# Kernel tuning notes

Hardware: AMD Instinct MI355X
Metric: run time of the kernel (lower is better)

Reference implementation:

```python
import jax, jax.numpy as jnp
import numpy as np

N = 100_000      # total nodes across batch of graphs
E = 1_600_000    # total directed edges
D = 128          # input feature dim
H = 128          # hidden dim
OUT = 10         # output classes
B = 500          # number of graphs (200 nodes each)
L_MID = 3        # GIN layers after the first (num_layers-2)


def setup_inputs() -> dict:
    key = jax.random.key(0)
    ks = jax.random.split(key, 24)
    s = np.float32(1.0 / np.sqrt(H))
    f32 = jnp.float32
    inp = {
        'node_features': jax.random.normal(ks[0], (N, D), f32),
        'edge_src': jax.random.randint(ks[1], (E,), 0, N, jnp.int32),
        'edge_dst': jax.random.randint(ks[2], (E,), 0, N, jnp.int32),
        'graph_ids': (jnp.arange(N) // (N // B)).astype(jnp.int32),
        # GIN eps per layer (torch init: zeros)
        'eps': jnp.zeros((4,), f32),
        # pre MLP (input layer): Linear(D,H) -> BN -> ReLU -> Linear(H,H), then pre_batchnorm
        'pre_W1': jax.random.normal(ks[3], (D, H), f32) * s,
        'pre_b1': jnp.zeros((H,), f32),
        'pre_g1': jnp.ones((H,), f32),
        'pre_bt1': jnp.zeros((H,), f32),
        'pre_W2': jax.random.normal(ks[4], (H, H), f32) * s,
        'pre_b2': jnp.zeros((H,), f32),
        'pre_gout': jnp.ones((H,), f32),
        'pre_btout': jnp.zeros((H,), f32),
        # middle GIN layers (stacked over L_MID)
        'mlp_W1': jax.random.normal(ks[5], (L_MID, H, H), f32) * s,
        'mlp_b1': jnp.zeros((L_MID, H), f32),
        'mlp_g1': jnp.ones((L_MID, H), f32),
        'mlp_bt1': jnp.zeros((L_MID, H), f32),
        'mlp_W2': jax.random.normal(ks[6], (L_MID, H, H), f32) * s,
        'mlp_b2': jnp.zeros((L_MID, H), f32),
        'bn_g': jnp.ones((L_MID, H), f32),
        'bn_bt': jnp.zeros((L_MID, H), f32),
        # per-layer prediction heads
        'pred_W0': jax.random.normal(ks[7], (D, OUT), f32) * s,
        'pred_b0': jnp.zeros((OUT,), f32),
        'pred_W': jax.random.normal(ks[8], (4, H, OUT), f32) * s,
        'pred_b': jnp.zeros((4, OUT), f32),
    }
    return inp


def _mlp_bn(x, W1, b1, g1, bt1, W2, b2, go, bo):
    # MLP(num_mlp_layers=2): Linear -> BN(eval) -> ReLU -> Linear, then outer BN(eval) -> ReLU
    h = jax.nn.relu(g1 * (x @ W1 + b1) + bt1)
    h = h @ W2 + b2
    return jax.nn.relu(go * h + bo)


def reference(node_features, edge_src, edge_dst, graph_ids, eps,
              pre_W1, pre_b1, pre_g1, pre_bt1, pre_W2, pre_b2, pre_gout, pre_btout,
              mlp_W1, mlp_b1, mlp_g1, mlp_bt1, mlp_W2, mlp_b2, bn_g, bn_bt,
              pred_W0, pred_b0, pred_W, pred_b):
    def agg(h):
        # sparse Adj @ h via gather + segment_sum (sum neighbor pooling, learn_eps=True -> no self loops)
        return jax.ops.segment_sum(h[edge_src], edge_dst, num_segments=N)

    h = node_features
    reps = [h]
    pooled = agg(h) + (1.0 + eps[0]) * h
    h = _mlp_bn(pooled, pre_W1, pre_b1, pre_g1, pre_bt1, pre_W2, pre_b2, pre_gout, pre_btout)
    reps.append(h)
    for i in range(L_MID):
        pooled = agg(h) + (1.0 + eps[i + 1]) * h
        h = _mlp_bn(pooled, mlp_W1[i], mlp_b1[i], mlp_g1[i], mlp_bt1[i],
                    mlp_W2[i], mlp_b2[i], bn_g[i], bn_bt[i])
        reps.append(h)

    # graph-level sum pooling + per-layer linear heads (dropout off in eval)
    score = jax.ops.segment_sum(reps[0], graph_ids, num_segments=B) @ pred_W0 + pred_b0
    for k in range(4):
        score = score + jax.ops.segment_sum(reps[k + 1], graph_ids, num_segments=B) @ pred_W[k] + pred_b[k]
    return score  # [B, OUT]
```

## Files before the change

kernel.cpp:

```cpp
#include <hip/hip_runtime.h>
#include <hip/hip_bf16.h>

#define NN 100000
#define EE 1600000
#define HH 128
#define OUTC 10
#define BB 500
#define GSZ 200
#define LDA 136

#define NBKT 782
#define BCAP 2560
#define EPB 4096
#define NBUCKB 391
#define NTILE128 782

typedef float f32x4 __attribute__((ext_vector_type(4)));
typedef __bf16 bf16x8 __attribute__((ext_vector_type(8)));

__device__ __forceinline__ float b2f(unsigned short u){
    unsigned int x = ((unsigned int)u) << 16;
    return __builtin_bit_cast(float, x);
}
__device__ __forceinline__ unsigned short f2b(float f){
    __hip_bfloat16 h = __float2bfloat16(f);
    return __builtin_bit_cast(unsigned short, h);
}

__global__ __launch_bounds__(256) void k_setup(const int* __restrict__ src, const int* __restrict__ dst,
                                               int* __restrict__ bucket_cursor, unsigned int* __restrict__ ebuf,
                                               const float* __restrict__ x, unsigned short* __restrict__ hA,
                                               float* __restrict__ G,
                                               const float* __restrict__ preW1, const float* __restrict__ preW2,
                                               const float* __restrict__ mlpW1, const float* __restrict__ mlpW2,
                                               unsigned short* __restrict__ Wbf){
    __shared__ __align__(16) unsigned int sval[EPB];
    __shared__ unsigned short sbkt[EPB];
    __shared__ int shist[NBKT];
    int t = threadIdx.x;
    int bid = blockIdx.x;

    if (bid < NBUCKB){
        int e0 = bid * EPB;
        for (int i = t; i < NBKT; i += 256) shist[i] = 0;
        __syncthreads();
        for (int i = t; i < EPB; i += 256){
            int e = e0 + i;
            if (e < EE){
                int d = dst[e];
                int b = d >> 7;
                sval[i] = ((unsigned)src[e] << 7) | (unsigned)(d & 127);
                sbkt[i] = (unsigned short)b;
                atomicAdd(&shist[b], 1);
            } else {
                sbkt[i] = 0xffff;
            }
        }
        __syncthreads();
        for (int i = t; i < NBKT; i += 256){
            int c = shist[i];
            shist[i] = c ? atomicAdd(&bucket_cursor[i], c) : 0;
        }
        __syncthreads();
        for (int i = t; i < EPB; i += 256){
            unsigned short b = sbkt[i];
            if (b != 0xffff){
                int pos = atomicAdd(&shist[b], 1);
                if (pos < BCAP) ebuf[(int)b * BCAP + pos] = sval[i];
            }
        }
    } else if (bid < NBUCKB + BB){
        float* r0 = (float*)sval;
        float* r1 = r0 + 256;
        int g = bid - NBUCKB;
        int f2 = t & 63;
        int rg = t >> 6;
        if (t < 128){
            #pragma unroll
            for (int k = 1; k < 5; ++k) G[(size_t)k*BB*128 + g*128 + t] = 0.f;
        }
        float a0 = 0.f, a1 = 0.f;
        for (int i = rg; i < GSZ; i += 4){
            int node = g*GSZ + i;
            float2 v = *(const float2*)(x + (size_t)node*128 + f2*2);
            a0 += v.x; a1 += v.y;
            unsigned int o = (unsigned)f2b(v.x) | ((unsigned)f2b(v.y) << 16);
            ((unsigned int*)hA)[(size_t)node*64 + f2] = o;
        }
        r0[t] = a0; r1[t] = a1;
        __syncthreads();
        if (t < 64){
            float s0 = r0[t] + r0[t+64] + r0[t+128] + r0[t+192];
            float s1 = r1[t] + r1[t+64] + r1[t+128] + r1[t+192];
            float2 v; v.x = s0; v.y = s1;
            *(float2*)(G + g*128 + t*2) = v;
        }
    } else {
        int idx = (bid - NBUCKB - BB)*256 + t;
        int w = idx >> 14;
        int rem = idx & 16383;
        int e = rem & 7;
        int chunk = rem >> 3;
        int m = chunk & 15;
        int q = (chunk >> 4) & 3;
        int kk = (chunk >> 6) & 3;
        int j = chunk >> 8;
        int n = j*16 + m;
        int k = kk*32 + q*8 + e;
        const float* s;
        if      (w == 0) s = preW1;
        else if (w == 1) s = preW2;
        else if (w <  5) s = mlpW1 + (w-2)*16384;
        else             s = mlpW2 + (w-5)*16384;
        Wbf[idx] = f2b(s[k*128 + n]);
    }
}

__global__ __launch_bounds__(1024) void k_bscan(const int* __restrict__ bucket_cursor,
                                                int* __restrict__ bucket_base, int* __restrict__ row_ptr){
    __shared__ int tmp[1024];
    int t = threadIdx.x;
    int v = (t < NBKT) ? min(bucket_cursor[t], BCAP) : 0;
    tmp[t] = v; __syncthreads();
    for (int off = 1; off < 1024; off <<= 1){
        int a = (t >= off) ? tmp[t - off] : 0;
        __syncthreads();
        tmp[t] += a;
        __syncthreads();
    }
    if (t < NBKT) bucket_base[t + 1] = tmp[t];
    if (t == 0){ bucket_base[0] = 0; row_ptr[NN] = EE; }
}

__global__ __launch_bounds__(256) void k_csr(const int* __restrict__ bucket_cursor, const int* __restrict__ bucket_base,
                                             const unsigned int* __restrict__ ebuf,
                                             int* __restrict__ row_ptr, int* __restrict__ col){
    __shared__ int cnt[128];
    __shared__ int pfx[128];
    int b = blockIdx.x;
    int t = threadIdx.x;
    int c    = min(bucket_cursor[b], BCAP);
    int base = bucket_base[b];
    if (t < 128) cnt[t] = 0;
    __syncthreads();
    const unsigned int* eb = ebuf + (size_t)b * BCAP;
    for (int i = t; i < c; i += 256) atomicAdd(&cnt[eb[i] & 127], 1);
    __syncthreads();
    if (t == 0){
        int run = 0;
        for (int i = 0; i < 128; ++i){ pfx[i] = run; run += cnt[i]; }
    }
    __syncthreads();
    int node0 = b * 128;
    if (t < 128 && node0 + t < NN) row_ptr[node0 + t] = base + pfx[t];
    if (t < 128) cnt[t] = pfx[t];
    __syncthreads();
    for (int i = t; i < c; i += 256){
        unsigned int v = eb[i];
        int pos = atomicAdd(&cnt[v & 127], 1);
        col[base + pos] = (int)(v >> 7);
    }
}

__device__ __forceinline__ void acc_u32(float* a, unsigned int v, int j){
    a[j]   += __builtin_bit_cast(float, v << 16);
    a[j+1] += __builtin_bit_cast(float, v & 0xffff0000u);
}
__device__ __forceinline__ void acc_u4(float* a, uint4 v){
    acc_u32(a, v.x, 0); acc_u32(a, v.y, 2); acc_u32(a, v.z, 4); acc_u32(a, v.w, 6);
}
__device__ __forceinline__ uint4 and4(uint4 v, unsigned mk){
    v.x &= mk; v.y &= mk; v.z &= mk; v.w &= mk; return v;
}

__global__ __launch_bounds__(256) void k_agg(const int* __restrict__ row_ptr, const int* __restrict__ col,
                                             const unsigned short* __restrict__ h,
                                             const float* __restrict__ eps, int l,
                                             unsigned short* __restrict__ pooled){
    int lane = threadIdx.x & 63;
    int wv   = threadIdx.x >> 6;
    int n    = blockIdx.x*4 + wv;
    int q = lane >> 4;
    int u = lane & 15;
    int beg = row_ptr[n], end = row_ptr[n+1];
    float a[8];
    #pragma unroll
    for (int j = 0; j < 8; ++j) a[j] = 0.f;

    int e = beg;
    for (; e + 16 <= end; e += 16){
        int c0 = col[e      + q];
        int c1 = col[e + 4  + q];
        int c2 = col[e + 8  + q];
        int c3 = col[e + 12 + q];
        uint4 v0 = *(const uint4*)(h + (size_t)c0*128 + u*8);
        uint4 v1 = *(const uint4*)(h + (size_t)c1*128 + u*8);
        uint4 v2 = *(const uint4*)(h + (size_t)c2*128 + u*8);
        uint4 v3 = *(const uint4*)(h + (size_t)c3*128 + u*8);
        acc_u4(a, v0); acc_u4(a, v1); acc_u4(a, v2); acc_u4(a, v3);
    }
    if (e < end){
        int last = end - 1;
        int i0 = e + q, i1 = e + 4 + q, i2 = e + 8 + q, i3 = e + 12 + q;
        int c0 = col[min(i0, last)];
        int c1 = col[min(i1, last)];
        int c2 = col[min(i2, last)];
        int c3 = col[min(i3, last)];
        uint4 v0 = *(const uint4*)(h + (size_t)c0*128 + u*8);
        uint4 v1 = *(const uint4*)(h + (size_t)c1*128 + u*8);
        uint4 v2 = *(const uint4*)(h + (size_t)c2*128 + u*8);
        uint4 v3 = *(const uint4*)(h + (size_t)c3*128 + u*8);
        v0 = and4(v0, (i0 < end) ? 0xffffffffu : 0u);
        v1 = and4(v1, (i1 < end) ? 0xffffffffu : 0u);
        v2 = and4(v2, (i2 < end) ? 0xffffffffu : 0u);
        v3 = and4(v3, (i3 < end) ? 0xffffffffu : 0u);
        acc_u4(a, v0); acc_u4(a, v1); acc_u4(a, v2); acc_u4(a, v3);
    }
    #pragma unroll
    for (int j = 0; j < 8; ++j){
        a[j] += __shfl_xor(a[j], 16, 64);
        a[j] += __shfl_xor(a[j], 32, 64);
    }
    if (q == 0){
        float ep = 1.0f + eps[l];
        uint4 hs = *(const uint4*)(h + (size_t)n*128 + u*8);
        a[0] += ep * __builtin_bit_cast(float, hs.x << 16);
        a[1] += ep * __builtin_bit_cast(float, hs.x & 0xffff0000u);
        a[2] += ep * __builtin_bit_cast(float, hs.y << 16);
        a[3] += ep * __builtin_bit_cast(float, hs.y & 0xffff0000u);
        a[4] += ep * __builtin_bit_cast(float, hs.z << 16);
        a[5] += ep * __builtin_bit_cast(float, hs.z & 0xffff0000u);
        a[6] += ep * __builtin_bit_cast(float, hs.w << 16);
        a[7] += ep * __builtin_bit_cast(float, hs.w & 0xffff0000u);
        uint4 o;
        o.x = (unsigned)f2b(a[0]) | ((unsigned)f2b(a[1]) << 16);
        o.y = (unsigned)f2b(a[2]) | ((unsigned)f2b(a[3]) << 16);
        o.z = (unsigned)f2b(a[4]) | ((unsigned)f2b(a[5]) << 16);
        o.w = (unsigned)f2b(a[6]) | ((unsigned)f2b(a[7]) << 16);
        *(uint4*)(pooled + (size_t)n*128 + u*8) = o;
    }
}

__device__ __forceinline__ void load_a(const unsigned short* __restrict__ Ain, int tile,
                                       int wv, int m, int q, bf16x8* dst){
    int node = tile*128 + wv*16 + m;
    bool valid = node < NN;
    const unsigned short* base = Ain + (size_t)(valid ? node : 0)*128 + q*8;
    #pragma unroll
    for (int kk = 0; kk < 4; ++kk){
        int4 v = *(const int4*)(base + kk*32);
        if (!valid) v = make_int4(0,0,0,0);
        dst[kk] = __builtin_bit_cast(bf16x8, v);
    }
}

__global__ __launch_bounds__(512, 2) void k_mlp(const unsigned short* __restrict__ Ain,
                                                unsigned short* __restrict__ Out,
                                                const unsigned short* __restrict__ Wf1,
                                                const unsigned short* __restrict__ Wf2,
                                                const float* __restrict__ b1v, const float* __restrict__ g1v,
                                                const float* __restrict__ bt1v,
                                                const float* __restrict__ b2v, const float* __restrict__ g2v,
                                                const float* __restrict__ bt2v,
                                                float* __restrict__ Gout){
    __shared__ __align__(16) unsigned short W1l[16384];
    __shared__ __align__(16) unsigned short W2l[16384];
    __shared__ __align__(16) unsigned short Ys[8][16*LDA];
    int t = threadIdx.x;
    int lane = t & 63, wv = t >> 6;
    int m = lane & 15, q = lane >> 4;
    #pragma unroll
    for (int i = t; i < 2048; i += 512){
        *(int4*)(&W1l[i*8]) = *(const int4*)(Wf1 + i*8);
        *(int4*)(&W2l[i*8]) = *(const int4*)(Wf2 + i*8);
    }
    __syncthreads();
    float ge1[8], ce1[8], ge2[8], ce2[8];
    #pragma unroll
    for (int j = 0; j < 8; ++j){
        int colc = j*16 + m;
        float gv1 = g1v[colc]; ge1[j] = gv1; ce1[j] = b1v[colc]*gv1 + bt1v[colc];
        float gv2 = g2v[colc]; ge2[j] = gv2; ce2[j] = b2v[colc]*gv2 + bt2v[colc];
    }
    unsigned short* Y = &Ys[wv][0];
    int tile = blockIdx.x;
    bf16x8 aN[4];
    if (tile < NTILE128) load_a(Ain, tile, wv, m, q, aN);
    while (tile < NTILE128){
        bf16x8 a[4];
        #pragma unroll
        for (int kk = 0; kk < 4; ++kk) a[kk] = aN[kk];
        int nxt = tile + gridDim.x;
        if (nxt < NTILE128) load_a(Ain, nxt, wv, m, q, aN);
        f32x4 acc[8];
        #pragma unroll
        for (int j = 0; j < 8; ++j) acc[j] = (f32x4){0.f,0.f,0.f,0.f};
        #pragma unroll
        for (int kk = 0; kk < 4; ++kk){
            #pragma unroll
            for (int j = 0; j < 8; ++j){
                bf16x8 b = *(const bf16x8*)(&W1l[((((j*4+kk)*4+q)*16)+m)*8]);
                acc[j] = __builtin_amdgcn_mfma_f32_16x16x32_bf16(a[kk], b, acc[j], 0, 0, 0);
            }
        }
        #pragma unroll
        for (int j = 0; j < 8; ++j){
            int colc = j*16 + m;
            #pragma unroll
            for (int r = 0; r < 4; ++r){
                float v = fmaxf(acc[j][r]*ge1[j] + ce1[j], 0.f);
                Y[(q*4 + r)*LDA + colc] = f2b(v);
            }
        }
        f32x4 acc2[8];
        #pragma unroll
        for (int j = 0; j < 8; ++j) acc2[j] = (f32x4){0.f,0.f,0.f,0.f};
        #pragma unroll
        for (int kk = 0; kk < 4; ++kk){
            bf16x8 ya = *(const bf16x8*)(&Y[m*LDA + kk*32 + q*8]);
            #pragma unroll
            for (int j = 0; j < 8; ++j){
                bf16x8 b = *(const bf16x8*)(&W2l[((((j*4+kk)*4+q)*16)+m)*8]);
                acc2[j] = __builtin_amdgcn_mfma_f32_16x16x32_bf16(ya, b, acc2[j], 0, 0, 0);
            }
        }
        #pragma unroll
        for (int j = 0; j < 8; ++j){
            int colc = j*16 + m;
            #pragma unroll
            for (int r = 0; r < 4; ++r){
                float v = fmaxf(acc2[j][r]*ge2[j] + ce2[j], 0.f);
                Y[(q*4 + r)*LDA + colc] = f2b(v);
            }
        }
        int row0 = tile*128 + wv*16;
        #pragma unroll
        for (int i = 0; i < 4; ++i){
            int idx = i*64 + lane;
            int r = idx >> 4, c = idx & 15;
            int nd = row0 + r;
            if (nd < NN)
                *(int4*)(Out + (size_t)nd*128 + c*8) = *(const int4*)(&Y[r*LDA + c*8]);
        }
        {
            float run0 = 0.f, run1 = 0.f;
            int curg = row0 / GSZ;
            for (int r = 0; r < 16; ++r){
                int nd = row0 + r;
                if (nd >= NN) break;
                int g = nd / GSZ;
                if (g != curg){
                    if (run0 != 0.f) atomicAdd(&Gout[curg*128 + lane*2], run0);
                    if (run1 != 0.f) atomicAdd(&Gout[curg*128 + lane*2 + 1], run1);
                    run0 = 0.f; run1 = 0.f; curg = g;
                }
                unsigned int v = *(const unsigned int*)(&Y[r*LDA + lane*2]);
                run0 += b2f((unsigned short)v);
                run1 += b2f((unsigned short)(v >> 16));
            }
            if (run0 != 0.f) atomicAdd(&Gout[curg*128 + lane*2], run0);
            if (run1 != 0.f) atomicAdd(&Gout[curg*128 + lane*2 + 1], run1);
        }
        tile = nxt;
    }
}

__global__ __launch_bounds__(256) void k_score(const float* __restrict__ G,
                                               const float* __restrict__ W0, const float* __restrict__ b0,
                                               const float* __restrict__ Wk, const float* __restrict__ bk,
                                               float* __restrict__ out){
    int id = blockIdx.x*256 + threadIdx.x;
    if (id >= BB*OUTC) return;
    int b = id / OUTC, o = id % OUTC;
    float s = b0[o];
    #pragma unroll
    for (int k = 0; k < 4; ++k) s += bk[k*OUTC + o];
    const float* g0 = G + b*128;
    for (int c = 0; c < 128; ++c) s += g0[c] * W0[c*OUTC + o];
    for (int k = 0; k < 4; ++k){
        const float* gk = G + (size_t)(k+1)*BB*128 + b*128;
        const float* wk = Wk + k*128*OUTC;
        for (int c = 0; c < 128; ++c) s += gk[c] * wk[c*OUTC + o];
    }
    out[id] = s;
}

extern "C" void kernel_launch(void* const* d_in, const int* in_sizes, int n_in,
                              void* d_out, int out_size, void* d_ws, size_t ws_size,
                              hipStream_t stream){
    const float* node_features = (const float*)d_in[0];
    const int*   edge_src  = (const int*)d_in[1];
    const int*   edge_dst  = (const int*)d_in[2];
    const float* eps       = (const float*)d_in[4];
    const float* pre_W1    = (const float*)d_in[5];
    const float* pre_b1    = (const float*)d_in[6];
    const float* pre_g1    = (const float*)d_in[7];
    const float* pre_bt1   = (const float*)d_in[8];
    const float* pre_W2    = (const float*)d_in[9];
    const float* pre_b2    = (const float*)d_in[10];
    const float* pre_gout  = (const float*)d_in[11];
    const float* pre_btout = (const float*)d_in[12];
    const float* mlp_W1    = (const float*)d_in[13];
    const float* mlp_b1    = (const float*)d_in[14];
    const float* mlp_g1    = (const float*)d_in[15];
    const float* mlp_bt1   = (const float*)d_in[16];
    const float* mlp_W2    = (const float*)d_in[17];
    const float* mlp_b2    = (const float*)d_in[18];
    const float* bn_g      = (const float*)d_in[19];
    const float* bn_bt     = (const float*)d_in[20];
    const float* pred_W0   = (const float*)d_in[21];
    const float* pred_b0   = (const float*)d_in[22];
    const float* pred_W    = (const float*)d_in[23];
    const float* pred_b    = (const float*)d_in[24];
    float* out = (float*)d_out;

    char* p = (char*)d_ws;
    auto alloc = [&](size_t bytes)->char*{
        char* r = p;
        p += (bytes + 255) & ~(size_t)255;
        return r;
    };
    int* bucket_cursor    = (int*)alloc((size_t)NBKT*4);
    int* bucket_base      = (int*)alloc((size_t)(NBKT+1)*4);
    int* row_ptr          = (int*)alloc((size_t)(NN+1)*4);
    int* col              = (int*)alloc((size_t)EE*4);
    unsigned int* ebuf    = (unsigned int*)alloc((size_t)NBKT*BCAP*4);
    unsigned short* Wbf   = (unsigned short*)alloc((size_t)8*128*128*2);
    unsigned short* hA    = (unsigned short*)alloc((size_t)NN*128*2);
    unsigned short* hB    = (unsigned short*)alloc((size_t)NN*128*2);
    unsigned short* pooled= (unsigned short*)alloc((size_t)NN*128*2);
    float* G              = (float*)alloc((size_t)5*BB*128*4);

    hipMemsetAsync(bucket_cursor, 0, (size_t)NBKT*4, stream);

    k_setup<<<NBUCKB + BB + 512, 256, 0, stream>>>(edge_src, edge_dst, bucket_cursor, ebuf,
                                                   node_features, hA, G,
                                                   pre_W1, pre_W2, mlp_W1, mlp_W2, Wbf);
    k_bscan<<<1, 1024, 0, stream>>>(bucket_cursor, bucket_base, row_ptr);
    k_csr<<<NBKT, 256, 0, stream>>>(bucket_cursor, bucket_base, ebuf, row_ptr, col);

    const unsigned short* hcur = hA;
    unsigned short* hnxt = hB;
    for (int l = 0; l < 4; ++l){
        k_agg<<<NN/4, 256, 0, stream>>>(row_ptr, col, hcur, eps, l, pooled);
        const unsigned short *W1t, *W2t;
        const float *b1,*g1,*bt1,*b2,*g2,*bt2;
        if (l == 0){
            W1t = Wbf;             W2t = Wbf + 16384;
            b1 = pre_b1; g1 = pre_g1; bt1 = pre_bt1;
            b2 = pre_b2; g2 = pre_gout; bt2 = pre_btout;
        } else {
            W1t = Wbf + (size_t)(2 + (l-1))*16384;
            W2t = Wbf + (size_t)(5 + (l-1))*16384;
            b1 = mlp_b1 + (l-1)*128; g1 = mlp_g1 + (l-1)*128; bt1 = mlp_bt1 + (l-1)*128;
            b2 = mlp_b2 + (l-1)*128; g2 = bn_g   + (l-1)*128; bt2 = bn_bt   + (l-1)*128;
        }
        k_mlp<<<256, 512, 0, stream>>>(pooled, hnxt, W1t, W2t,
                                       b1, g1, bt1, b2, g2, bt2,
                                       G + (size_t)(l+1)*BB*128);
        const unsigned short* tmp = hnxt;
        hnxt = (unsigned short*)hcur;
        hcur = tmp;
    }
    k_score<<<(BB*OUTC + 255)/256, 256, 0, stream>>>(G, pred_W0, pred_b0, pred_W, pred_b, out);
}
```

Before: 558.3 us.

## Fold BN scale into weights, widen gather batch, swizzle MLP LDS, separate pooling

The BatchNorm gamma is folded into the bf16 weight conversion, so the MLP epilogue only adds a precomputed bias. MFMA operands are swapped so each lane holds four consecutive output columns, allowing packed 8-byte stores and an XOR-swizzled LDS intermediate without padding. The aggregation loop gathers 32 neighbours per iteration and accumulates pairs with bf16 dot2 instructions to add ILP. Graph pooling moves out of the MLP kernel's atomics into a separate per-graph reduction kernel, which costs an extra launch and a re-read of h per layer.

```diff
diff --git a/kernel.cpp b/kernel.cpp
--- a/kernel.cpp
+++ b/kernel.cpp
@@ -7,7 +7,6 @@
 #define OUTC 10
 #define BB 500
 #define GSZ 200
-#define LDA 136
 
 #define NBKT 782
 #define BCAP 2560
@@ -17,6 +16,7 @@
 
 typedef float f32x4 __attribute__((ext_vector_type(4)));
 typedef __bf16 bf16x8 __attribute__((ext_vector_type(8)));
+typedef __bf16 bf16x2 __attribute__((ext_vector_type(2)));
 
 __device__ __forceinline__ float b2f(unsigned short u){
     unsigned int x = ((unsigned int)u) << 16;
@@ -33,6 +33,8 @@
                                                float* __restrict__ G,
                                                const float* __restrict__ preW1, const float* __restrict__ preW2,
                                                const float* __restrict__ mlpW1, const float* __restrict__ mlpW2,
+                                               const float* __restrict__ preG1, const float* __restrict__ preGout,
+                                               const float* __restrict__ mlpG1, const float* __restrict__ bnG,
                                                unsigned short* __restrict__ Wbf){
     __shared__ __align__(16) unsigned int sval[EPB];
     __shared__ unsigned short sbkt[EPB];
@@ -75,10 +77,6 @@
         int g = bid - NBUCKB;
         int f2 = t & 63;
         int rg = t >> 6;
-        if (t < 128){
-            #pragma unroll
-            for (int k = 1; k < 5; ++k) G[(size_t)k*BB*128 + g*128 + t] = 0.f;
-        }
         float a0 = 0.f, a1 = 0.f;
         for (int i = rg; i < GSZ; i += 4){
             int node = g*GSZ + i;
@@ -107,12 +105,12 @@
         int j = chunk >> 8;
         int n = j*16 + m;
         int k = kk*32 + q*8 + e;
-        const float* s;
-        if      (w == 0) s = preW1;
-        else if (w == 1) s = preW2;
-        else if (w <  5) s = mlpW1 + (w-2)*16384;
-        else             s = mlpW2 + (w-5)*16384;
-        Wbf[idx] = f2b(s[k*128 + n]);
+        const float* s; const float* gv;
+        if      (w == 0){ s = preW1;                 gv = preG1; }
+        else if (w == 1){ s = preW2;                 gv = preGout; }
+        else if (w <  5){ s = mlpW1 + (w-2)*16384;   gv = mlpG1 + (w-2)*128; }
+        else            { s = mlpW2 + (w-5)*16384;   gv = bnG   + (w-5)*128; }
+        Wbf[idx] = f2b(s[k*128 + n] * gv[n]);
     }
 }
 
@@ -171,6 +169,48 @@
 }
 __device__ __forceinline__ uint4 and4(uint4 v, unsigned mk){
     v.x &= mk; v.y &= mk; v.z &= mk; v.w &= mk; return v;
+}
+
+#if __has_builtin(__builtin_amdgcn_fdot2_f32_bf16) && __has_builtin(__builtin_amdgcn_perm)
+#define HAVE_DOT2 1
+__device__ __forceinline__ void pair_comp(float* a, unsigned va, unsigned vb, int j){
+    unsigned lo = __builtin_amdgcn_perm(vb, va, 0x05040100u);
+    unsigned hi = __builtin_amdgcn_perm(vb, va, 0x07060302u);
+    bf16x2 one = __builtin_bit_cast(bf16x2, 0x3F803F80u);
+    a[j]   = __builtin_amdgcn_fdot2_f32_bf16(__builtin_bit_cast(bf16x2, lo), one, a[j],   false);
+    a[j+1] = __builtin_amdgcn_fdot2_f32_bf16(__builtin_bit_cast(bf16x2, hi), one, a[j+1], false);
+}
+__device__ __forceinline__ void pair_acc(float* a, uint4 va, uint4 vb){
+    pair_comp(a, va.x, vb.x, 0);
+    pair_comp(a, va.y, vb.y, 2);
+    pair_comp(a, va.z, vb.z, 4);
+    pair_comp(a, va.w, vb.w, 6);
+}
+#else
+__device__ __forceinline__ void pair_acc(float* a, uint4 va, uint4 vb){
+    acc_u4(a, va); acc_u4(a, vb);
+}
+#endif
+
+template<bool MASK>
+__device__ __forceinline__ void agg32(const int* __restrict__ col, const unsigned short* __restrict__ h,
+                                      int e, int end, int q, int u, float* a){
+    int last = end - 1;
+    uint4 v[8];
+    int idx[8];
+    #pragma unroll
+    for (int t = 0; t < 8; ++t){
+        int i = e + 4*t + q;
+        idx[t] = i;
+        int c = col[MASK ? min(i, last) : i];
+        v[t] = *(const uint4*)(h + (size_t)c*128 + u*8);
+    }
+    if (MASK){
+        #pragma unroll
+        for (int t = 0; t < 8; ++t) v[t] = and4(v[t], idx[t] < end ? 0xffffffffu : 0u);
+    }
+    #pragma unroll
+    for (int t = 0; t < 8; t += 2) pair_acc(a, v[t], v[t+1]);
 }
 
 __global__ __launch_bounds__(256) void k_agg(const int* __restrict__ row_ptr, const int* __restrict__ col,
@@ -188,34 +228,9 @@
     for (int j = 0; j < 8; ++j) a[j] = 0.f;
 
     int e = beg;
-    for (; e + 16 <= end; e += 16){
-        int c0 = col[e      + q];
-        int c1 = col[e + 4  + q];
-        int c2 = col[e + 8  + q];
-        int c3 = col[e + 12 + q];
-        uint4 v0 = *(const uint4*)(h + (size_t)c0*128 + u*8);
-        uint4 v1 = *(const uint4*)(h + (size_t)c1*128 + u*8);
-        uint4 v2 = *(const uint4*)(h + (size_t)c2*128 + u*8);
-        uint4 v3 = *(const uint4*)(h + (size_t)c3*128 + u*8);
-        acc_u4(a, v0); acc_u4(a, v1); acc_u4(a, v2); acc_u4(a, v3);
-    }
-    if (e < end){
-        int last = end - 1;
-        int i0 = e + q, i1 = e + 4 + q, i2 = e + 8 + q, i3 = e + 12 + q;
-        int c0 = col[min(i0, last)];
-        int c1 = col[min(i1, last)];
-        int c2 = col[min(i2, last)];
-        int c3 = col[min(i3, last)];
-        uint4 v0 = *(const uint4*)(h + (size_t)c0*128 + u*8);
-        uint4 v1 = *(const uint4*)(h + (size_t)c1*128 + u*8);
-        uint4 v2 = *(const uint4*)(h + (size_t)c2*128 + u*8);
-        uint4 v3 = *(const uint4*)(h + (size_t)c3*128 + u*8);
-        v0 = and4(v0, (i0 < end) ? 0xffffffffu : 0u);
-        v1 = and4(v1, (i1 < end) ? 0xffffffffu : 0u);
-        v2 = and4(v2, (i2 < end) ? 0xffffffffu : 0u);
-        v3 = and4(v3, (i3 < end) ? 0xffffffffu : 0u);
-        acc_u4(a, v0); acc_u4(a, v1); acc_u4(a, v2); acc_u4(a, v3);
-    }
+    for (; e + 32 <= end; e += 32) agg32<false>(col, h, e, end, q, u, a);
+    if (e < end)                   agg32<true >(col, h, e, end, q, u, a);
+
     #pragma unroll
     for (int j = 0; j < 8; ++j){
         a[j] += __shfl_xor(a[j], 16, 64);
@@ -261,28 +276,33 @@
                                                 const float* __restrict__ b1v, const float* __restrict__ g1v,
                                                 const float* __restrict__ bt1v,
                                                 const float* __restrict__ b2v, const float* __restrict__ g2v,
-                                                const float* __restrict__ bt2v,
-                                                float* __restrict__ Gout){
+                                                const float* __restrict__ bt2v){
     __shared__ __align__(16) unsigned short W1l[16384];
     __shared__ __align__(16) unsigned short W2l[16384];
-    __shared__ __align__(16) unsigned short Ys[8][16*LDA];
+    __shared__ __align__(16) unsigned short Ys[8][2048];
     int t = threadIdx.x;
     int lane = t & 63, wv = t >> 6;
     int m = lane & 15, q = lane >> 4;
-    #pragma unroll
     for (int i = t; i < 2048; i += 512){
         *(int4*)(&W1l[i*8]) = *(const int4*)(Wf1 + i*8);
         *(int4*)(&W2l[i*8]) = *(const int4*)(Wf2 + i*8);
     }
     __syncthreads();
-    float ge1[8], ce1[8], ge2[8], ce2[8];
+    f32x4 cb1[8], cb2[8];
     #pragma unroll
     for (int j = 0; j < 8; ++j){
-        int colc = j*16 + m;
-        float gv1 = g1v[colc]; ge1[j] = gv1; ce1[j] = b1v[colc]*gv1 + bt1v[colc];
-        float gv2 = g2v[colc]; ge2[j] = gv2; ce2[j] = b2v[colc]*gv2 + bt2v[colc];
-    }
-    unsigned short* Y = &Ys[wv][0];
+        int c0 = j*16 + q*4;
+        f32x4 bb = *(const f32x4*)(b1v + c0);
+        f32x4 gg = *(const f32x4*)(g1v + c0);
+        f32x4 tt = *(const f32x4*)(bt1v + c0);
+        cb1[j] = bb*gg + tt;
+        bb = *(const f32x4*)(b2v + c0);
+        gg = *(const f32x4*)(g2v + c0);
+        tt = *(const f32x4*)(bt2v + c0);
+        cb2[j] = bb*gg + tt;
+    }
+    unsigned char* Yb = (unsigned char*)(&Ys[wv][0]);
+    int swz = (m & 7) << 4;
     int tile = blockIdx.x;
     bf16x8 aN[4];
     if (tile < NTILE128) load_a(Ain, tile, wv, m, q, aN);
@@ -300,68 +320,67 @@
             #pragma unroll
             for (int j = 0; j < 8; ++j){
                 bf16x8 b = *(const bf16x8*)(&W1l[((((j*4+kk)*4+q)*16)+m)*8]);
-                acc[j] = __builtin_amdgcn_mfma_f32_16x16x32_bf16(a[kk], b, acc[j], 0, 0, 0);
+                acc[j] = __builtin_amdgcn_mfma_f32_16x16x32_bf16(b, a[kk], acc[j], 0, 0, 0);
             }
         }
         #pragma unroll
         for (int j = 0; j < 8; ++j){
-            int colc = j*16 + m;
-            #pragma unroll
-            for (int r = 0; r < 4; ++r){
-                float v = fmaxf(acc[j][r]*ge1[j] + ce1[j], 0.f);
-                Y[(q*4 + r)*LDA + colc] = f2b(v);
-            }
+            f32x4 y = acc[j] + cb1[j];
+            uint2 pk;
+            pk.x = (unsigned)f2b(fmaxf(y[0], 0.f)) | ((unsigned)f2b(fmaxf(y[1], 0.f)) << 16);
+            pk.y = (unsigned)f2b(fmaxf(y[2], 0.f)) | ((unsigned)f2b(fmaxf(y[3], 0.f)) << 16);
+            int off = (m*256 + j*32 + q*8) ^ swz;
+            *(uint2*)(Yb + off) = pk;
         }
         f32x4 acc2[8];
         #pragma unroll
         for (int j = 0; j < 8; ++j) acc2[j] = (f32x4){0.f,0.f,0.f,0.f};
         #pragma unroll
         for (int kk = 0; kk < 4; ++kk){
-            bf16x8 ya = *(const bf16x8*)(&Y[m*LDA + kk*32 + q*8]);
+            int off = (m*256 + kk*64 + q*16) ^ swz;
+            bf16x8 ya = *(const bf16x8*)(Yb + off);
             #pragma unroll
             for (int j = 0; j < 8; ++j){
                 bf16x8 b = *(const bf16x8*)(&W2l[((((j*4+kk)*4+q)*16)+m)*8]);
-                acc2[j] = __builtin_amdgcn_mfma_f32_16x16x32_bf16(ya, b, acc2[j], 0, 0, 0);
+                acc2[j] = __builtin_amdgcn_mfma_f32_16x16x32_bf16(b, ya, acc2[j], 0, 0, 0);
             }
         }
+        int node = tile*128 + wv*16 + m;
+        bool valid = node < NN;
+        unsigned short* orow = Out + (size_t)node*128;
         #pragma unroll
         for (int j = 0; j < 8; ++j){
-            int colc = j*16 + m;
-            #pragma unroll
-            for (int r = 0; r < 4; ++r){
-                float v = fmaxf(acc2[j][r]*ge2[j] + ce2[j], 0.f);
-                Y[(q*4 + r)*LDA + colc] = f2b(v);
-            }
-        }
-        int row0 = tile*128 + wv*16;
-        #pragma unroll
-        for (int i = 0; i < 4; ++i){
-            int idx = i*64 + lane;
-            int r = idx >> 4, c = idx & 15;
-            int nd = row0 + r;
-            if (nd < NN)
-                *(int4*)(Out + (size_t)nd*128 + c*8) = *(const int4*)(&Y[r*LDA + c*8]);
-        }
-        {
-            float run0 = 0.f, run1 = 0.f;
-            int curg = row0 / GSZ;
-            for (int r = 0; r < 16; ++r){
-                int nd = row0 + r;
-                if (nd >= NN) break;
-                int g = nd / GSZ;
-                if (g != curg){
-                    if (run0 != 0.f) atomicAdd(&Gout[curg*128 + lane*2], run0);
-                    if (run1 != 0.f) atomicAdd(&Gout[curg*128 + lane*2 + 1], run1);
-                    run0 = 0.f; run1 = 0.f; curg = g;
-                }
-                unsigned int v = *(const unsigned int*)(&Y[r*LDA + lane*2]);
-                run0 += b2f((unsigned short)v);
-                run1 += b2f((unsigned short)(v >> 16));
-            }
-            if (run0 != 0.f) atomicAdd(&Gout[curg*128 + lane*2], run0);
-            if (run1 != 0.f) atomicAdd(&Gout[curg*128 + lane*2 + 1], run1);
+            f32x4 z = acc2[j] + cb2[j];
+            uint2 pk;
+            pk.x = (unsigned)f2b(fmaxf(z[0], 0.f)) | ((unsigned)f2b(fmaxf(z[1], 0.f)) << 16);
+            pk.y = (unsigned)f2b(fmaxf(z[2], 0.f)) | ((unsigned)f2b(fmaxf(z[3], 0.f)) << 16);
+            if (valid) *(uint2*)(orow + j*16 + q*4) = pk;
         }
         tile = nxt;
+    }
+}
+
+__global__ __launch_bounds__(256) void k_pool(const unsigned short* __restrict__ h,
+                                              float* __restrict__ Gout){
+    __shared__ float red[512];
+    int g = blockIdx.x;
+    int t = threadIdx.x;
+    int f2 = t & 63;
+    int rg = t >> 6;
+    const unsigned int* hu = (const unsigned int*)h;
+    float a0 = 0.f, a1 = 0.f;
+    for (int i = rg; i < GSZ; i += 4){
+        unsigned int v = hu[(size_t)(g*GSZ + i)*64 + f2];
+        a0 += b2f((unsigned short)v);
+        a1 += b2f((unsigned short)(v >> 16));
+    }
+    red[t] = a0; red[t + 256] = a1;
+    __syncthreads();
+    if (t < 64){
+        float s0 = red[t]     + red[t+64]  + red[t+128] + red[t+192];
+        float s1 = red[t+256] + red[t+320] + red[t+384] + red[t+448];
+        float2 v; v.x = s0; v.y = s1;
+        *(float2*)(Gout + g*128 + t*2) = v;
     }
 }
 
@@ -435,7 +454,8 @@
 
     k_setup<<<NBUCKB + BB + 512, 256, 0, stream>>>(edge_src, edge_dst, bucket_cursor, ebuf,
                                                    node_features, hA, G,
-                                                   pre_W1, pre_W2, mlp_W1, mlp_W2, Wbf);
+                                                   pre_W1, pre_W2, mlp_W1, mlp_W2,
+                                                   pre_g1, pre_gout, mlp_g1, bn_g, Wbf);
     k_bscan<<<1, 1024, 0, stream>>>(bucket_cursor, bucket_base, row_ptr);
     k_csr<<<NBKT, 256, 0, stream>>>(bucket_cursor, bucket_base, ebuf, row_ptr, col);
 
@@ -456,8 +476,8 @@
             b2 = mlp_b2 + (l-1)*128; g2 = bn_g   + (l-1)*128; bt2 = bn_bt   + (l-1)*128;
         }
         k_mlp<<<256, 512, 0, stream>>>(pooled, hnxt, W1t, W2t,
-                                       b1, g1, bt1, b2, g2, bt2,
-                                       G + (size_t)(l+1)*BB*128);
+                                       b1, g1, bt1, b2, g2, bt2);
+        k_pool<<<BB, 256, 0, stream>>>(hnxt, G + (size_t)(l+1)*BB*128);
         const unsigned short* tmp = hnxt;
         hnxt = (unsigned short*)hcur;
         hcur = tmp;
```

Result: slower. 865.6 us (+55.0%).
